# Optimization experiments

Hardware: AMD Instinct MI355X
Metric: run time of the kernel (lower is better)

Reference implementation:

```python
import jax, jax.numpy as jnp
import numpy as np

B, N, F = 4, 4096, 32
NG = 14  # number of gate graph-convs in GCNLSTM_Cell with memory state


def setup_inputs() -> dict:
    key = jax.random.key(0)
    ks = jax.random.split(key, 7)
    x = jax.random.normal(ks[0], (B, N, F), jnp.float32)
    h = jax.random.normal(ks[1], (B, N, F), jnp.float32)
    c = jax.random.normal(ks[2], (B, N, F), jnp.float32)
    m = jax.random.normal(ks[3], (B, N, F), jnp.float32)
    # weighted dense adjacency, scaled so row sums are O(1)
    adj = jax.random.uniform(ks[4], (N, N), jnp.float32) / N
    # 14 WeightedGraphConv layers: Dense F -> 2F (single FeedForward layer, no relu)
    W = jax.random.normal(ks[5], (NG, F, 2 * F), jnp.float32) * (1.0 / np.sqrt(F))
    b = jnp.zeros((NG, 2 * F), jnp.float32)
    return {"x": x, "h": h, "c": c, "m": m, "adj": adj, "W": W, "b": b}


def _gcn(ax, W, b):
    # ax: [B,N,F] = adj @ state (precomputed); Dense to 2F then GLU split.
    z = ax @ W + b  # [B,N,2F]
    ls, rs = jnp.split(z, 2, axis=-1)
    return ls * jax.nn.sigmoid(rs)


def reference(x, h, c, m, adj, W, b):
    # shared graph aggregation for x and h (adj is the same for all gates)
    ax = jnp.einsum('nm,bmf->bnf', adj, x)  # [B,N,F]
    ah = jnp.einsum('nm,bmf->bnf', adj, h)

    fx = _gcn(ax, W[0], b[0]); fh = _gcn(ah, W[1], b[1])
    ix = _gcn(ax, W[2], b[2]); ih = _gcn(ah, W[3], b[3])
    cx = _gcn(ax, W[4], b[4]); ch = _gcn(ah, W[5], b[5])
    ox = _gcn(ax, W[6], b[6]); oh = _gcn(ah, W[7], b[7])

    f = jax.nn.sigmoid(fx + fh)
    i = jax.nn.sigmoid(ix + ih)
    o = jax.nn.sigmoid(ox + oh)
    c_new = f * c + i * jnp.tanh(cx + ch)
    h1 = o * jnp.tanh(c_new)

    # memory-state block (6 more graph convs on h1 and m)
    ah1 = jnp.einsum('nm,bmf->bnf', adj, h1)
    am = jnp.einsum('nm,bmf->bnf', adj, m)
    sa_ih = _gcn(ah1, W[8], b[8]);  sa_im = _gcn(am, W[9], b[9])
    sa_gh = _gcn(ah1, W[10], b[10]); sa_gm = _gcn(am, W[11], b[11])
    sa_oh = _gcn(ah1, W[12], b[12]); sa_om = _gcn(am, W[13], b[13])

    i2 = jax.nn.sigmoid(sa_ih + sa_im)
    g = jax.nn.sigmoid(sa_gh + sa_gm)
    o2 = jax.nn.sigmoid(sa_oh + sa_om)
    m_new = i2 * m + (1.0 - i2) * g
    h_new = m_new * o2
    return h_new, c_new, m_new
```

## Files before the change

### kernel.cpp

```cpp
#include <hip/hip_runtime.h>
#include <stdint.h>

typedef __attribute__((ext_vector_type(4))) float f32x4;
typedef __attribute__((ext_vector_type(8))) short s16x8;

#define BB 4
#define NN 4096
#define FF 32
#define BNF (BB*NN*FF)

typedef __attribute__((address_space(3))) void       as3_void;
typedef const __attribute__((address_space(1))) void as1_cvoid;

static __device__ __forceinline__ float bf2f(uint16_t u) {
    union { uint32_t i; float f; } v; v.i = ((uint32_t)u) << 16; return v.f;
}
static __device__ __forceinline__ uint16_t f2bf(float f) {
    union { float f; uint32_t i; } v; v.f = f;
    uint32_t r = v.i + 0x7FFFu + ((v.i >> 16) & 1u);
    return (uint16_t)(r >> 16);
}
static __device__ __forceinline__ float sig_acc(float x) { return 1.0f / (1.0f + expf(-x)); }

__global__ __launch_bounds__(256) void prep_kernel(
    const float* __restrict__ adj, uint16_t* __restrict__ adjb, int cvtN,
    const float* __restrict__ Wf, uint16_t* __restrict__ Wp,
    const float* __restrict__ x, const float* __restrict__ h,
    const float* __restrict__ m,
    uint16_t* __restrict__ P, uint16_t* __restrict__ P2)
{
    int bid = blockIdx.x;
    int t = threadIdx.x;

    if (bid < cvtN) {
        size_t i = ((size_t)bid * 256 + t) * 8;
        float4 v0 = *(const float4*)(adj + i);
        float4 v1 = *(const float4*)(adj + i + 4);
        union { uint4 u; uint16_t e[8]; } o;
        o.e[0] = f2bf(v0.x); o.e[1] = f2bf(v0.y); o.e[2] = f2bf(v0.z); o.e[3] = f2bf(v0.w);
        o.e[4] = f2bf(v1.x); o.e[5] = f2bf(v1.y); o.e[6] = f2bf(v1.z); o.e[7] = f2bf(v1.w);
        *(uint4*)(adjb + i) = o.u;
        return;
    }
    bid -= cvtN;

    if (bid < 112) {
        int idx = bid * 256 + t;
        int g   = idx >> 11;
        int k   = (idx >> 6) & 31;
        int col = idx & 63;
        uint16_t v = f2bf(Wf[idx]);
        int gp = g >> 1;
        int sl = ((g & 1) << 2) | (k >> 3);
        int ph = sl ^ (col & 7);
        Wp[((gp * 64 + col) * 64) + ph * 8 + (k & 7)] = v;
        return;
    }
    bid -= 112;

    const float* src; uint16_t* dst; int rowbase, b, n0;
    if (bid < 512) {
        int tensor = bid >> 8;
        src = tensor ? h : x; dst = P; rowbase = tensor * 128;
        b = (bid >> 6) & 3; n0 = (bid & 63) * 64;
    } else {
        int q = bid - 512;
        src = m; dst = P2; rowbase = 128;
        b = q >> 6; n0 = (q & 63) * 64;
    }
    __shared__ uint16_t tl[32][65];
    {
        int i = t >> 2, ch = t & 3;
        size_t idx = ((size_t)(b * NN + n0 + i)) * FF + ch * 8;
        float4 v0 = *(const float4*)(src + idx);
        float4 v1 = *(const float4*)(src + idx + 4);
        uint16_t e[8] = { f2bf(v0.x), f2bf(v0.y), f2bf(v0.z), f2bf(v0.w),
                          f2bf(v1.x), f2bf(v1.y), f2bf(v1.z), f2bf(v1.w) };
        #pragma unroll
        for (int k = 0; k < 8; k++) tl[ch * 8 + k][i] = e[k];
    }
    __syncthreads();
    {
        int f = t >> 3, ch = t & 7;
        union { uint4 u; uint16_t e[8]; } v;
        #pragma unroll
        for (int k = 0; k < 8; k++) v.e[k] = tl[f][ch * 8 + k];
        size_t row = (size_t)(rowbase + b * 32 + f);
        *(uint4*)(dst + row * NN + n0 + ch * 8) = v.u;
    }
}

__global__ __launch_bounds__(256, 2) void mega1_kernel(
    const void* __restrict__ Av,
    const uint16_t* __restrict__ P,
    const uint16_t* __restrict__ Wp,
    const float* __restrict__ bf_,
    const float* __restrict__ cf,
    float* __restrict__ cnew, uint16_t* __restrict__ S2t, int isf32A)
{
    __shared__ __align__(16) uint16_t aLb[4][32 * 32];
    __shared__ __align__(16) uint16_t bLb[4][64 * 32];
    __shared__ float    AL[64 * 33];
    __shared__ float    SX[4][64][9];
    __shared__ uint16_t H1[32 * 18];

    int t = threadIdx.x;
    int bid = blockIdx.x;
    int b = bid >> 7, n0 = (bid & 127) * 32;
    int lane = t & 63, w = t >> 6;
    int lm = lane & 15, lk = lane >> 4;
    int j = lm, kg = lk;
    int ej = t & 15, erow = (t >> 4) & 15;

    const uint16_t* A16 = (const uint16_t*)Av;
    const float*    Af  = (const float*)Av;

    float cv[2][2];
    #pragma unroll
    for (int gh = 0; gh < 2; gh++)
        #pragma unroll
        for (int hh = 0; hh < 2; hh++)
            cv[gh][hh] = cf[((size_t)(b * NN + n0 + gh * 16 + erow)) * FF + ej + hh * 16];

    int aq0 = t >> 7,        ap0 = (t & 127) * 16;
    int ar0 = ap0 >> 6,      asl0 = ((ap0 >> 4) & 3) ^ ((ar0 >> 1) & 3);
    int gs1 = t + 256;
    int aq1 = gs1 >> 7,      ap1 = (gs1 & 127) * 16;
    int ar1 = ap1 >> 6,      asl1 = ((ap1 >> 4) & 3) ^ ((ar1 >> 1) & 3);
    int bpos = t * 16;
    int brow = bpos >> 6;
    int bslot = ((bpos >> 4) & 3) ^ ((brow >> 1) & 3);
    int bcrow = brow + ((brow < 32) ? b * 32 : 96 + b * 32);
    int rB = w * 16 + lm; int swB = (lk ^ ((rB >> 1) & 3)) * 8;
    int swA = (lk ^ ((lm >> 1) & 3)) * 8;

    f32x4 acc0 = {}, acc1 = {};
    for (int kk = 0; kk < 4096; kk += 128) {
        if (!isf32A) {
            __builtin_amdgcn_global_load_lds(
                (as1_cvoid*)(A16 + (size_t)(n0 + ar0) * 4096 + kk + aq0 * 32 + asl0 * 8),
                (as3_void*)((char*)aLb[aq0] + ap0), 16, 0, 0);
            __builtin_amdgcn_global_load_lds(
                (as1_cvoid*)(A16 + (size_t)(n0 + ar1) * 4096 + kk + aq1 * 32 + asl1 * 8),
                (as3_void*)((char*)aLb[aq1] + ap1), 16, 0, 0);
        } else {
            union { uint4 u; uint16_t e[8]; } sa0, sa1;
            {
                size_t aidx = (size_t)(n0 + ar0) * 4096 + kk + aq0 * 32 + asl0 * 8;
                union { uint4 u[2]; float f[8]; } va;
                va.u[0] = *(const uint4*)(Af + aidx);
                va.u[1] = *(const uint4*)(Af + aidx + 4);
                #pragma unroll
                for (int k = 0; k < 8; k++) sa0.e[k] = f2bf(va.f[k]);
            }
            {
                size_t aidx = (size_t)(n0 + ar1) * 4096 + kk + aq1 * 32 + asl1 * 8;
                union { uint4 u[2]; float f[8]; } va;
                va.u[0] = *(const uint4*)(Af + aidx);
                va.u[1] = *(const uint4*)(Af + aidx + 4);
                #pragma unroll
                for (int k = 0; k < 8; k++) sa1.e[k] = f2bf(va.f[k]);
            }
            *(uint4*)((char*)aLb[aq0] + ap0) = sa0.u;
            *(uint4*)((char*)aLb[aq1] + ap1) = sa1.u;
        }
        #pragma unroll
        for (int q = 0; q < 4; q++) {
            size_t bidx = (size_t)bcrow * 4096 + kk + q * 32 + bslot * 8;
            __builtin_amdgcn_global_load_lds((as1_cvoid*)(P + bidx),
                (as3_void*)((char*)bLb[q] + bpos), 16, 0, 0);
        }
        __syncthreads();
        #pragma unroll
        for (int q = 0; q < 4; q++) {
            s16x8 af0 = *(const s16x8*)(aLb[q] + lm * 32 + swA);
            s16x8 af1 = *(const s16x8*)(aLb[q] + (16 + lm) * 32 + swA);
            s16x8 bf  = *(const s16x8*)(bLb[q] + rB * 32 + swB);
            acc0 = __builtin_amdgcn_mfma_f32_16x16x32_bf16(af0, bf, acc0, 0, 0, 0);
            acc1 = __builtin_amdgcn_mfma_f32_16x16x32_bf16(af1, bf, acc1, 0, 0, 0);
        }
        __syncthreads();
    }

    {
        int cp = w * 16 + lm;
        #pragma unroll
        for (int r = 0; r < 4; r++) {
            AL[cp * 33 + lk * 4 + r]      = acc0[r];
            AL[cp * 33 + 16 + lk * 4 + r] = acc1[r];
        }
    }
    __syncthreads();

    for (int gh = 0; gh < 2; gh++) {
        int colb = gh * 16;
        s16x8 a_ax, a_ah;
        #pragma unroll
        for (int e = 0; e < 8; e++) {
            int k = kg * 8 + e;
            a_ax[e] = (short)f2bf(AL[k * 33 + colb + j]);
            a_ah[e] = (short)f2bf(AL[(32 + k) * 33 + colb + j]);
        }
        {
            int p = w;
            int g0 = p * 2, g1 = p * 2 + 1;
            f32x4 ac0[4] = {}, ac1[4] = {};
            #pragma unroll
            for (int ct = 0; ct < 4; ct++) {
                int col = ct * 16 + j;
                int ph0 = (kg)     ^ (col & 7);
                int ph1 = (4 + kg) ^ (col & 7);
                s16x8 b0 = *(const s16x8*)(Wp + (p * 64 + col) * 64 + ph0 * 8);
                s16x8 b1 = *(const s16x8*)(Wp + (p * 64 + col) * 64 + ph1 * 8);
                ac0[ct] = __builtin_amdgcn_mfma_f32_16x16x32_bf16(a_ax, b0, ac0[ct], 0, 0, 0);
                ac1[ct] = __builtin_amdgcn_mfma_f32_16x16x32_bf16(a_ah, b1, ac1[ct], 0, 0, 0);
            }
            #pragma unroll
            for (int hh = 0; hh < 2; hh++)
                #pragma unroll
                for (int r = 0; r < 4; r++) {
                    float z0l = ac0[hh][r]     + bf_[g0 * 64 + hh * 16 + j];
                    float z0r = ac0[2 + hh][r] + bf_[g0 * 64 + 32 + hh * 16 + j];
                    float z1l = ac1[hh][r]     + bf_[g1 * 64 + hh * 16 + j];
                    float z1r = ac1[2 + hh][r] + bf_[g1 * 64 + 32 + hh * 16 + j];
                    SX[p][lane][hh * 4 + r] = z0l * sig_acc(z0r) + z1l * sig_acc(z1r);
                }
        }
        __syncthreads();
        {
            int pl = ((erow >> 2) << 4) | ej;
            int ridx = erow & 3;
            #pragma unroll
            for (int hh = 0; hh < 2; hh++) {
                float s0 = SX[0][pl][hh * 4 + ridx];
                float s1 = SX[1][pl][hh * 4 + ridx];
                float s2 = SX[2][pl][hh * 4 + ridx];
                float s3 = SX[3][pl][hh * 4 + ridx];
                float fg = sig_acc(s0), ig = sig_acc(s1);
                float cc = tanhf(s2),   og = sig_acc(s3);
                float cn = fg * cv[gh][hh] + ig * cc;
                size_t gidx = ((size_t)(b * NN + n0 + gh * 16 + erow)) * FF + ej + hh * 16;
                cnew[gidx] = cn;
                H1[(ej + hh * 16) * 18 + erow] = f2bf(og * tanhf(cn));
            }
        }
        __syncthreads();
        if (t < 64) {
            int f = t >> 1, half = t & 1;
            union { uint4 u; uint16_t e[8]; } v;
            #pragma unroll
            for (int k = 0; k < 8; k++) v.e[k] = H1[f * 18 + half * 8 + k];
            *(uint4*)(S2t + ((size_t)(b * 32 + f)) * NN + n0 + gh * 16 + half * 8) = v.u;
        }
        __syncthreads();
    }
}

__global__ __launch_bounds__(256, 2) void mega2_kernel(
    const void* __restrict__ Av,
    const uint16_t* __restrict__ P2,
    const uint16_t* __restrict__ Wp,
    const float* __restrict__ bf_,
    const float* __restrict__ mf,
    float* __restrict__ hnew, float* __restrict__ mnew, int isf32A)
{
    __shared__ __align__(16) uint16_t aLb[4][32 * 32];
    __shared__ __align__(16) uint16_t bLb[4][64 * 32];
    __shared__ float AL[64 * 33];
    __shared__ float SX[3][64][9];

    int t = threadIdx.x;
    int bid = blockIdx.x;
    int b = bid >> 7, n0 = (bid & 127) * 32;
    int lane = t & 63, w = t >> 6;
    int lm = lane & 15, lk = lane >> 4;
    int j = lm, kg = lk;
    int ej = t & 15, erow = (t >> 4) & 15;

    const uint16_t* A16 = (const uint16_t*)Av;
    const float*    Af  = (const float*)Av;

    float mv[2][2];
    #pragma unroll
    for (int gh = 0; gh < 2; gh++)
        #pragma unroll
        for (int hh = 0; hh < 2; hh++)
            mv[gh][hh] = mf[((size_t)(b * NN + n0 + gh * 16 + erow)) * FF + ej + hh * 16];

    int aq0 = t >> 7,        ap0 = (t & 127) * 16;
    int ar0 = ap0 >> 6,      asl0 = ((ap0 >> 4) & 3) ^ ((ar0 >> 1) & 3);
    int gs1 = t + 256;
    int aq1 = gs1 >> 7,      ap1 = (gs1 & 127) * 16;
    int ar1 = ap1 >> 6,      asl1 = ((ap1 >> 4) & 3) ^ ((ar1 >> 1) & 3);
    int bpos = t * 16;
    int brow = bpos >> 6;
    int bslot = ((bpos >> 4) & 3) ^ ((brow >> 1) & 3);
    int bcrow = brow + ((brow < 32) ? b * 32 : 96 + b * 32);
    int rB = w * 16 + lm; int swB = (lk ^ ((rB >> 1) & 3)) * 8;
    int swA = (lk ^ ((lm >> 1) & 3)) * 8;

    f32x4 acc0 = {}, acc1 = {};
    for (int kk = 0; kk < 4096; kk += 128) {
        if (!isf32A) {
            __builtin_amdgcn_global_load_lds(
                (as1_cvoid*)(A16 + (size_t)(n0 + ar0) * 4096 + kk + aq0 * 32 + asl0 * 8),
                (as3_void*)((char*)aLb[aq0] + ap0), 16, 0, 0);
            __builtin_amdgcn_global_load_lds(
                (as1_cvoid*)(A16 + (size_t)(n0 + ar1) * 4096 + kk + aq1 * 32 + asl1 * 8),
                (as3_void*)((char*)aLb[aq1] + ap1), 16, 0, 0);
        } else {
            union { uint4 u; uint16_t e[8]; } sa0, sa1;
            {
                size_t aidx = (size_t)(n0 + ar0) * 4096 + kk + aq0 * 32 + asl0 * 8;
                union { uint4 u[2]; float f[8]; } va;
                va.u[0] = *(const uint4*)(Af + aidx);
                va.u[1] = *(const uint4*)(Af + aidx + 4);
                #pragma unroll
                for (int k = 0; k < 8; k++) sa0.e[k] = f2bf(va.f[k]);
            }
            {
                size_t aidx = (size_t)(n0 + ar1) * 4096 + kk + aq1 * 32 + asl1 * 8;
                union { uint4 u[2]; float f[8]; } va;
                va.u[0] = *(const uint4*)(Af + aidx);
                va.u[1] = *(const uint4*)(Af + aidx + 4);
                #pragma unroll
                for (int k = 0; k < 8; k++) sa1.e[k] = f2bf(va.f[k]);
            }
            *(uint4*)((char*)aLb[aq0] + ap0) = sa0.u;
            *(uint4*)((char*)aLb[aq1] + ap1) = sa1.u;
        }
        #pragma unroll
        for (int q = 0; q < 4; q++) {
            size_t bidx = (size_t)bcrow * 4096 + kk + q * 32 + bslot * 8;
            __builtin_amdgcn_global_load_lds((as1_cvoid*)(P2 + bidx),
                (as3_void*)((char*)bLb[q] + bpos), 16, 0, 0);
        }
        __syncthreads();
        #pragma unroll
        for (int q = 0; q < 4; q++) {
            s16x8 af0 = *(const s16x8*)(aLb[q] + lm * 32 + swA);
            s16x8 af1 = *(const s16x8*)(aLb[q] + (16 + lm) * 32 + swA);
            s16x8 bf  = *(const s16x8*)(bLb[q] + rB * 32 + swB);
            acc0 = __builtin_amdgcn_mfma_f32_16x16x32_bf16(af0, bf, acc0, 0, 0, 0);
            acc1 = __builtin_amdgcn_mfma_f32_16x16x32_bf16(af1, bf, acc1, 0, 0, 0);
        }
        __syncthreads();
    }

    {
        int cp = w * 16 + lm;
        #pragma unroll
        for (int r = 0; r < 4; r++) {
            AL[cp * 33 + lk * 4 + r]      = acc0[r];
            AL[cp * 33 + 16 + lk * 4 + r] = acc1[r];
        }
    }
    __syncthreads();

    for (int gh = 0; gh < 2; gh++) {
        int colb = gh * 16;
        if (w < 3) {
            s16x8 a_h1, a_m;
            #pragma unroll
            for (int e = 0; e < 8; e++) {
                int k = kg * 8 + e;
                a_h1[e] = (short)f2bf(AL[k * 33 + colb + j]);
                a_m[e]  = (short)f2bf(AL[(32 + k) * 33 + colb + j]);
            }
            const uint16_t* WpG = Wp + 4 * 64 * 64;
            const float*    bG  = bf_ + 512;
            int p = w;
            int g0 = p * 2, g1 = p * 2 + 1;
            f32x4 ac0[4] = {}, ac1[4] = {};
            #pragma unroll
            for (int ct = 0; ct < 4; ct++) {
                int col = ct * 16 + j;
                int ph0 = (kg)     ^ (col & 7);
                int ph1 = (4 + kg) ^ (col & 7);
                s16x8 b0 = *(const s16x8*)(WpG + (p * 64 + col) * 64 + ph0 * 8);
                s16x8 b1 = *(const s16x8*)(WpG + (p * 64 + col) * 64 + ph1 * 8);
                ac0[ct] = __builtin_amdgcn_mfma_f32_16x16x32_bf16(a_h1, b0, ac0[ct], 0, 0, 0);
                ac1[ct] = __builtin_amdgcn_mfma_f32_16x16x32_bf16(a_m, b1, ac1[ct], 0, 0, 0);
            }
            #pragma unroll
            for (int hh = 0; hh < 2; hh++)
                #pragma unroll
                for (int r = 0; r < 4; r++) {
                    float z0l = ac0[hh][r]     + bG[g0 * 64 + hh * 16 + j];
                    float z0r = ac0[2 + hh][r] + bG[g0 * 64 + 32 + hh * 16 + j];
                    float z1l = ac1[hh][r]     + bG[g1 * 64 + hh * 16 + j];
                    float z1r = ac1[2 + hh][r] + bG[g1 * 64 + 32 + hh * 16 + j];
                    SX[p][lane][hh * 4 + r] = z0l * sig_acc(z0r) + z1l * sig_acc(z1r);
                }
        }
        __syncthreads();
        {
            int pl = ((erow >> 2) << 4) | ej;
            int ridx = erow & 3;
            #pragma unroll
            for (int hh = 0; hh < 2; hh++) {
                float s0 = SX[0][pl][hh * 4 + ridx];
                float s1 = SX[1][pl][hh * 4 + ridx];
                float s2 = SX[2][pl][hh * 4 + ridx];
                float i2 = sig_acc(s0);
                float gg = sig_acc(s1);
                float o2 = sig_acc(s2);
                float mn = i2 * mv[gh][hh] + (1.0f - i2) * gg;
                size_t gidx = ((size_t)(b * NN + n0 + gh * 16 + erow)) * FF + ej + hh * 16;
                mnew[gidx] = mn;
                hnew[gidx] = mn * o2;
            }
        }
        __syncthreads();
    }
}

extern "C" void kernel_launch(void* const* d_in, const int* in_sizes, int n_in,
                              void* d_out, int out_size, void* d_ws, size_t ws_size,
                              hipStream_t stream) {
    (void)in_sizes; (void)n_in; (void)out_size;
    const float* x   = (const float*)d_in[0];
    const float* h   = (const float*)d_in[1];
    const float* c   = (const float*)d_in[2];
    const float* m   = (const float*)d_in[3];
    const float* adj = (const float*)d_in[4];
    const float* W   = (const float*)d_in[5];
    const float* bb  = (const float*)d_in[6];
    float* out = (float*)d_out;

    char* ws = (char*)d_ws;
    int haveAdjb = ws_size >= (size_t)(40u << 20);
    uint16_t* adjb = (uint16_t*)ws;
    size_t pOff = haveAdjb ? (size_t)(32u << 20) : 0;
    uint16_t* P    = (uint16_t*)(ws + pOff);
    uint16_t* P2   = (uint16_t*)(ws + pOff + (2u << 20));
    uint16_t* Wp   = (uint16_t*)(ws + pOff + (4u << 20));

    if (ws_size < (6u << 20)) return;

    const void* Agemm = haveAdjb ? (const void*)adjb : (const void*)adj;
    int isf32A = haveAdjb ? 0 : 1;
    int cvtN = haveAdjb ? 8192 : 0;

    prep_kernel<<<cvtN + 112 + 768, 256, 0, stream>>>(adj, adjb, cvtN, W, Wp, x, h, m, P, P2);

    mega1_kernel<<<512, 256, 0, stream>>>(Agemm, P, Wp, bb, c, out + BNF, P2, isf32A);
    mega2_kernel<<<512, 256, 0, stream>>>(Agemm, P2, Wp, bb, m, out, out + 2 * BNF, isf32A);
}
```

Measured before the change: 172.9 us.

## Double-buffer LDS tiles in both mega kernels' adjacency GEMM loop

Doubles the LDS staging buffers for the adjacency and projected-state tiles and prefetches the next K-chunk with direct global-to-LDS loads while the current chunk feeds MFMA. A partial vmcnt wait plus raw barriers replaces the two __syncthreads per iteration, so global-load latency is meant to overlap with compute. The LDS footprint roughly doubles, which may limit the two-blocks-per-CU occupancy target. The fp32 adjacency fallback path stays single-buffered and now uses plain loads for the B tile.

```diff
diff --git a/kernel.cpp b/kernel.cpp
--- a/kernel.cpp
+++ b/kernel.cpp
@@ -98,8 +98,8 @@
     const float* __restrict__ cf,
     float* __restrict__ cnew, uint16_t* __restrict__ S2t, int isf32A)
 {
-    __shared__ __align__(16) uint16_t aLb[4][32 * 32];
-    __shared__ __align__(16) uint16_t bLb[4][64 * 32];
+    __shared__ __align__(16) uint16_t aLb[2][4][32 * 32];
+    __shared__ __align__(16) uint16_t bLb[2][4][64 * 32];
     __shared__ float    AL[64 * 33];
     __shared__ float    SX[4][64][9];
     __shared__ uint16_t H1[32 * 18];
@@ -135,15 +135,50 @@
     int swA = (lk ^ ((lm >> 1) & 3)) * 8;
 
     f32x4 acc0 = {}, acc1 = {};
-    for (int kk = 0; kk < 4096; kk += 128) {
-        if (!isf32A) {
-            __builtin_amdgcn_global_load_lds(
-                (as1_cvoid*)(A16 + (size_t)(n0 + ar0) * 4096 + kk + aq0 * 32 + asl0 * 8),
-                (as3_void*)((char*)aLb[aq0] + ap0), 16, 0, 0);
-            __builtin_amdgcn_global_load_lds(
-                (as1_cvoid*)(A16 + (size_t)(n0 + ar1) * 4096 + kk + aq1 * 32 + asl1 * 8),
-                (as3_void*)((char*)aLb[aq1] + ap1), 16, 0, 0);
-        } else {
+
+    if (!isf32A) {
+        #define ISSUE1(kk, d)                                                          \
+        {                                                                              \
+            __builtin_amdgcn_global_load_lds(                                          \
+                (as1_cvoid*)(A16 + (size_t)(n0 + ar0) * 4096 + (kk) + aq0 * 32 + asl0 * 8), \
+                (as3_void*)((char*)aLb[d][aq0] + ap0), 16, 0, 0);                      \
+            __builtin_amdgcn_global_load_lds(                                          \
+                (as1_cvoid*)(A16 + (size_t)(n0 + ar1) * 4096 + (kk) + aq1 * 32 + asl1 * 8), \
+                (as3_void*)((char*)aLb[d][aq1] + ap1), 16, 0, 0);                      \
+            _Pragma("unroll")                                                          \
+            for (int q = 0; q < 4; q++)                                                \
+                __builtin_amdgcn_global_load_lds(                                      \
+                    (as1_cvoid*)(P + (size_t)bcrow * 4096 + (kk) + q * 32 + bslot * 8),\
+                    (as3_void*)((char*)bLb[d][q] + bpos), 16, 0, 0);                   \
+        }
+        #define COMPUTE1(d)                                                            \
+        {                                                                              \
+            _Pragma("unroll")                                                          \
+            for (int q = 0; q < 4; q++) {                                              \
+                s16x8 af0 = *(const s16x8*)(aLb[d][q] + lm * 32 + swA);                \
+                s16x8 af1 = *(const s16x8*)(aLb[d][q] + (16 + lm) * 32 + swA);         \
+                s16x8 bf  = *(const s16x8*)(bLb[d][q] + rB * 32 + swB);                \
+                acc0 = __builtin_amdgcn_mfma_f32_16x16x32_bf16(af0, bf, acc0, 0, 0, 0);\
+                acc1 = __builtin_amdgcn_mfma_f32_16x16x32_bf16(af1, bf, acc1, 0, 0, 0);\
+            }                                                                          \
+        }
+        ISSUE1(0, 0);
+        int cur = 0;
+        for (int it = 0; it < 31; ++it) {
+            ISSUE1((it + 1) << 7, cur ^ 1);
+            asm volatile("s_waitcnt vmcnt(6)" ::: "memory");
+            __builtin_amdgcn_s_barrier();
+            COMPUTE1(cur);
+            __builtin_amdgcn_s_barrier();
+            cur ^= 1;
+        }
+        asm volatile("s_waitcnt vmcnt(0)" ::: "memory");
+        __builtin_amdgcn_s_barrier();
+        COMPUTE1(cur);
+        #undef ISSUE1
+        #undef COMPUTE1
+    } else {
+        for (int kk = 0; kk < 4096; kk += 128) {
             union { uint4 u; uint16_t e[8]; } sa0, sa1;
             {
                 size_t aidx = (size_t)(n0 + ar0) * 4096 + kk + aq0 * 32 + asl0 * 8;
@@ -161,27 +196,29 @@
                 #pragma unroll
                 for (int k = 0; k < 8; k++) sa1.e[k] = f2bf(va.f[k]);
             }
-            *(uint4*)((char*)aLb[aq0] + ap0) = sa0.u;
-            *(uint4*)((char*)aLb[aq1] + ap1) = sa1.u;
-        }
-        #pragma unroll
-        for (int q = 0; q < 4; q++) {
-            size_t bidx = (size_t)bcrow * 4096 + kk + q * 32 + bslot * 8;
-            __builtin_amdgcn_global_load_lds((as1_cvoid*)(P + bidx),
-                (as3_void*)((char*)bLb[q] + bpos), 16, 0, 0);
-        }
-        __syncthreads();
-        #pragma unroll
-        for (int q = 0; q < 4; q++) {
-            s16x8 af0 = *(const s16x8*)(aLb[q] + lm * 32 + swA);
-            s16x8 af1 = *(const s16x8*)(aLb[q] + (16 + lm) * 32 + swA);
-            s16x8 bf  = *(const s16x8*)(bLb[q] + rB * 32 + swB);
-            acc0 = __builtin_amdgcn_mfma_f32_16x16x32_bf16(af0, bf, acc0, 0, 0, 0);
-            acc1 = __builtin_amdgcn_mfma_f32_16x16x32_bf16(af1, bf, acc1, 0, 0, 0);
-        }
-        __syncthreads();
-    }
-
+            *(uint4*)((char*)aLb[0][aq0] + ap0) = sa0.u;
+            *(uint4*)((char*)aLb[0][aq1] + ap1) = sa1.u;
+            #pragma unroll
+            for (int q = 0; q < 4; q++) {
+                size_t bidx = (size_t)bcrow * 4096 + kk + q * 32 + bslot * 8;
+                union { uint4 u; } sb;
+                sb.u = *(const uint4*)(P + bidx);
+                *(uint4*)((char*)bLb[0][q] + bpos) = sb.u;
+            }
+            __syncthreads();
+            #pragma unroll
+            for (int q = 0; q < 4; q++) {
+                s16x8 af0 = *(const s16x8*)(aLb[0][q] + lm * 32 + swA);
+                s16x8 af1 = *(const s16x8*)(aLb[0][q] + (16 + lm) * 32 + swA);
+                s16x8 bf  = *(const s16x8*)(bLb[0][q] + rB * 32 + swB);
+                acc0 = __builtin_amdgcn_mfma_f32_16x16x32_bf16(af0, bf, acc0, 0, 0, 0);
+                acc1 = __builtin_amdgcn_mfma_f32_16x16x32_bf16(af1, bf, acc1, 0, 0, 0);
+            }
+            __syncthreads();
+        }
+    }
+
+    __syncthreads();
     {
         int cp = w * 16 + lm;
         #pragma unroll
@@ -264,8 +301,8 @@
     const float* __restrict__ mf,
     float* __restrict__ hnew, float* __restrict__ mnew, int isf32A)
 {
-    __shared__ __align__(16) uint16_t aLb[4][32 * 32];
-    __shared__ __align__(16) uint16_t bLb[4][64 * 32];
+    __shared__ __align__(16) uint16_t aLb[2][4][32 * 32];
+    __shared__ __align__(16) uint16_t bLb[2][4][64 * 32];
     __shared__ float AL[64 * 33];
     __shared__ float SX[3][64][9];
 
@@ -300,15 +337,50 @@
     int swA = (lk ^ ((lm >> 1) & 3)) * 8;
 
     f32x4 acc0 = {}, acc1 = {};
-    for (int kk = 0; kk < 4096; kk += 128) {
-        if (!isf32A) {
-            __builtin_amdgcn_global_load_lds(
-                (as1_cvoid*)(A16 + (size_t)(n0 + ar0) * 4096 + kk + aq0 * 32 + asl0 * 8),
-                (as3_void*)((char*)aLb[aq0] + ap0), 16, 0, 0);
-            __builtin_amdgcn_global_load_lds(
-                (as1_cvoid*)(A16 + (size_t)(n0 + ar1) * 4096 + kk + aq1 * 32 + asl1 * 8),
-                (as3_void*)((char*)aLb[aq1] + ap1), 16, 0, 0);
-        } else {
+
+    if (!isf32A) {
+        #define ISSUE2(kk, d)                                                          \
+        {                                                                              \
+            __builtin_amdgcn_global_load_lds(                                          \
+                (as1_cvoid*)(A16 + (size_t)(n0 + ar0) * 4096 + (kk) + aq0 * 32 + asl0 * 8), \
+                (as3_void*)((char*)aLb[d][aq0] + ap0), 16, 0, 0);                      \
+            __builtin_amdgcn_global_load_lds(                                          \
+                (as1_cvoid*)(A16 + (size_t)(n0 + ar1) * 4096 + (kk) + aq1 * 32 + asl1 * 8), \
+                (as3_void*)((char*)aLb[d][aq1] + ap1), 16, 0, 0);                      \
+            _Pragma("unroll")                                                          \
+            for (int q = 0; q < 4; q++)                                                \
+                __builtin_amdgcn_global_load_lds(                                      \
+                    (as1_cvoid*)(P2 + (size_t)bcrow * 4096 + (kk) + q * 32 + bslot * 8),\
+                    (as3_void*)((char*)bLb[d][q] + bpos), 16, 0, 0);                   \
+        }
+        #define COMPUTE2(d)                                                            \
+        {                                                                              \
+            _Pragma("unroll")                                                          \
+            for (int q = 0; q < 4; q++) {                                              \
+                s16x8 af0 = *(const s16x8*)(aLb[d][q] + lm * 32 + swA);                \
+                s16x8 af1 = *(const s16x8*)(aLb[d][q] + (16 + lm) * 32 + swA);         \
+                s16x8 bf  = *(const s16x8*)(bLb[d][q] + rB * 32 + swB);                \
+                acc0 = __builtin_amdgcn_mfma_f32_16x16x32_bf16(af0, bf, acc0, 0, 0, 0);\
+                acc1 = __builtin_amdgcn_mfma_f32_16x16x32_bf16(af1, bf, acc1, 0, 0, 0);\
+            }                                                                          \
+        }
+        ISSUE2(0, 0);
+        int cur = 0;
+        for (int it = 0; it < 31; ++it) {
+            ISSUE2((it + 1) << 7, cur ^ 1);
+            asm volatile("s_waitcnt vmcnt(6)" ::: "memory");
+            __builtin_amdgcn_s_barrier();
+            COMPUTE2(cur);
+            __builtin_amdgcn_s_barrier();
+            cur ^= 1;
+        }
+        asm volatile("s_waitcnt vmcnt(0)" ::: "memory");
+        __builtin_amdgcn_s_barrier();
+        COMPUTE2(cur);
+        #undef ISSUE2
+        #undef COMPUTE2
+    } else {
+        for (int kk = 0; kk < 4096; kk += 128) {
             union { uint4 u; uint16_t e[8]; } sa0, sa1;
             {
                 size_t aidx = (size_t)(n0 + ar0) * 4096 + kk + aq0 * 32 + asl0 * 8;
@@ -326,27 +398,29 @@
                 #pragma unroll
                 for (int k = 0; k < 8; k++) sa1.e[k] = f2bf(va.f[k]);
             }
-            *(uint4*)((char*)aLb[aq0] + ap0) = sa0.u;
-            *(uint4*)((char*)aLb[aq1] + ap1) = sa1.u;
-        }
-        #pragma unroll
-        for (int q = 0; q < 4; q++) {
-            size_t bidx = (size_t)bcrow * 4096 + kk + q * 32 + bslot * 8;
-            __builtin_amdgcn_global_load_lds((as1_cvoid*)(P2 + bidx),
-                (as3_void*)((char*)bLb[q] + bpos), 16, 0, 0);
-        }
-        __syncthreads();
-        #pragma unroll
-        for (int q = 0; q < 4; q++) {
-            s16x8 af0 = *(const s16x8*)(aLb[q] + lm * 32 + swA);
-            s16x8 af1 = *(const s16x8*)(aLb[q] + (16 + lm) * 32 + swA);
-            s16x8 bf  = *(const s16x8*)(bLb[q] + rB * 32 + swB);
-            acc0 = __builtin_amdgcn_mfma_f32_16x16x32_bf16(af0, bf, acc0, 0, 0, 0);
-            acc1 = __builtin_amdgcn_mfma_f32_16x16x32_bf16(af1, bf, acc1, 0, 0, 0);
-        }
-        __syncthreads();
-    }
-
+            *(uint4*)((char*)aLb[0][aq0] + ap0) = sa0.u;
+            *(uint4*)((char*)aLb[0][aq1] + ap1) = sa1.u;
+            #pragma unroll
+            for (int q = 0; q < 4; q++) {
+                size_t bidx = (size_t)bcrow * 4096 + kk + q * 32 + bslot * 8;
+                union { uint4 u; } sb;
+                sb.u = *(const uint4*)(P2 + bidx);
+                *(uint4*)((char*)bLb[0][q] + bpos) = sb.u;
+            }
+            __syncthreads();
+            #pragma unroll
+            for (int q = 0; q < 4; q++) {
+                s16x8 af0 = *(const s16x8*)(aLb[0][q] + lm * 32 + swA);
+                s16x8 af1 = *(const s16x8*)(aLb[0][q] + (16 + lm) * 32 + swA);
+                s16x8 bf  = *(const s16x8*)(bLb[0][q] + rB * 32 + swB);
+                acc0 = __builtin_amdgcn_mfma_f32_16x16x32_bf16(af0, bf, acc0, 0, 0, 0);
+                acc1 = __builtin_amdgcn_mfma_f32_16x16x32_bf16(af1, bf, acc1, 0, 0, 0);
+            }
+            __syncthreads();
+        }
+    }
+
+    __syncthreads();
     {
         int cp = w * 16 + lm;
         #pragma unroll
```

Result: no change. 171.0 us (-1.1%).
